# Optimization experiments

Hardware: AMD Instinct MI355X
Metric: run time of the kernel (lower is better)

The kernel has to match this reference:

```python
import jax, jax.numpy as jnp
import numpy as np

D_MODEL = 512
N_HEADS = 8
D_HEAD = D_MODEL // N_HEADS


def setup_inputs() -> dict:
    key = jax.random.key(0)
    ks = jax.random.split(key, 11)
    B, T = 4, 2048
    s = 1.0 / np.sqrt(D_MODEL)
    inp = {
        "Q": jax.random.normal(ks[0], (B, T, D_MODEL), jnp.float32),
        "K": jax.random.normal(ks[1], (B, T, D_MODEL), jnp.float32),
        "V": jax.random.normal(ks[2], (B, T, D_MODEL), jnp.float32),
        "W_q": jax.random.normal(ks[3], (D_MODEL, D_MODEL), jnp.float32) * s,
        "b_q": jnp.zeros((D_MODEL,), jnp.float32),
        "W_k": jax.random.normal(ks[4], (D_MODEL, D_MODEL), jnp.float32) * s,
        "b_k": jnp.zeros((D_MODEL,), jnp.float32),
        "W_v": jax.random.normal(ks[5], (D_MODEL, D_MODEL), jnp.float32) * s,
        "b_v": jnp.zeros((D_MODEL,), jnp.float32),
        "W_o": jax.random.normal(ks[6], (D_MODEL, D_MODEL), jnp.float32) * s,
        "b_o": jnp.zeros((D_MODEL,), jnp.float32),
    }
    return inp


def reference(Q, K, V, W_q, b_q, W_k, b_k, W_v, b_v, W_o, b_o):
    B, Tq, _ = Q.shape
    Tk = K.shape[1]
    # projections (torch Linear: x @ W.T + b)
    q = (Q @ W_q.T + b_q).reshape(B, Tq, N_HEADS, D_HEAD).transpose(0, 2, 1, 3)
    k = (K @ W_k.T + b_k).reshape(B, Tk, N_HEADS, D_HEAD).transpose(0, 2, 1, 3)
    v = (V @ W_v.T + b_v).reshape(B, Tk, N_HEADS, D_HEAD).transpose(0, 2, 1, 3)
    # scaled dot-product attention (mask=None path)
    scores = jnp.einsum("bhqd,bhkd->bhqk", q, k) / np.sqrt(D_HEAD).astype(np.float32)
    attn = jax.nn.softmax(scores, axis=-1)
    ctx = jnp.einsum("bhqk,bhkd->bhqd", attn, v)  # (B,h,Tq,d_v)
    ctx = ctx.transpose(0, 2, 1, 3).reshape(B, Tq, D_MODEL)
    out = ctx @ W_o.T + b_o
    return out, attn
```

## Files before the change

### kernel.cpp

```cpp
#include <hip/hip_runtime.h>
#include <math.h>

#define T_SEQ 2048
#define DM 512
#define NH 8
#define BATCH 4

typedef _Float16 f16;
typedef _Float16 f16x8 __attribute__((ext_vector_type(8)));
typedef _Float16 f16x4 __attribute__((ext_vector_type(4)));
typedef float f32x4 __attribute__((ext_vector_type(4)));

__device__ __forceinline__ f32x4 mfma16(f16x8 a, f16x8 b, f32x4 c) {
    return __builtin_amdgcn_mfma_f32_16x16x32_f16(a, b, c, 0, 0, 0);
}

__device__ __forceinline__ void cvt_f16x16(const float4& x0, const float4& x1,
                                           const float4& x2, const float4& x3,
                                           f16* dst) {
    f16x8 h0, h1;
    h0[0] = x0.x; h0[1] = x0.y; h0[2] = x0.z; h0[3] = x0.w;
    h0[4] = x1.x; h0[5] = x1.y; h0[6] = x1.z; h0[7] = x1.w;
    h1[0] = x2.x; h1[1] = x2.y; h1[2] = x2.z; h1[3] = x2.w;
    h1[4] = x3.x; h1[5] = x3.y; h1[6] = x3.z; h1[7] = x3.w;
    *(f16x8*)dst = h0; *(f16x8*)(dst + 8) = h1;
}

template <int XMODE, int OUTMODE>
__global__ __launch_bounds__(256)
void proj_kernel(const void* __restrict__ Xv, const float* __restrict__ W,
                 const float* __restrict__ bias, void* __restrict__ outv,
                 float scale)
{
    __shared__ char smem[18432];
    f16 (*As)[72] = (f16(*)[72])smem;
    f16 (*Bs)[72] = (f16(*)[72])(smem + 9216);

    const int tid  = threadIdx.x;
    const int lane = tid & 63;
    const int w    = tid >> 6;
    const int m    = lane & 15;
    const int quad = lane >> 4;
    const int m_off = (w & 1) * 32;
    const int n_off = (w >> 1) * 32;
    const int m0 = blockIdx.x << 6;
    const int n0 = blockIdx.y << 6;

    const int r = tid >> 2;
    const int c = (tid & 3) << 4;

    f32x4 acc[2][2] = {};

    const float* wrow = W + (size_t)(n0 + r) * 512 + c;

    float4 ax0, ax1, ax2, ax3;
    f16x8  ah0, ah1;
    float4 bx0, bx1, bx2, bx3;

    if (XMODE == 0) {
        const float* xr = (const float*)Xv + (size_t)(m0 + r) * 512 + c;
        ax0 = ((const float4*)xr)[0]; ax1 = ((const float4*)xr)[1];
        ax2 = ((const float4*)xr)[2]; ax3 = ((const float4*)xr)[3];
    } else {
        const f16x8* xr = (const f16x8*)((const f16*)Xv + (size_t)(m0 + r) * 512 + c);
        ah0 = xr[0]; ah1 = xr[1];
    }
    bx0 = ((const float4*)wrow)[0]; bx1 = ((const float4*)wrow)[1];
    bx2 = ((const float4*)wrow)[2]; bx3 = ((const float4*)wrow)[3];

    for (int k0 = 0; k0 < 512; k0 += 64) {
        __syncthreads();
        if (XMODE == 0) {
            cvt_f16x16(ax0, ax1, ax2, ax3, &As[r][c]);
        } else {
            *(f16x8*)&As[r][c] = ah0; *(f16x8*)&As[r][c + 8] = ah1;
        }
        cvt_f16x16(bx0, bx1, bx2, bx3, &Bs[r][c]);
        if (k0 + 64 < 512) {
            if (XMODE == 0) {
                const float* xr = (const float*)Xv + (size_t)(m0 + r) * 512 + k0 + 64 + c;
                ax0 = ((const float4*)xr)[0]; ax1 = ((const float4*)xr)[1];
                ax2 = ((const float4*)xr)[2]; ax3 = ((const float4*)xr)[3];
            } else {
                const f16x8* xr = (const f16x8*)((const f16*)Xv +
                                  (size_t)(m0 + r) * 512 + k0 + 64 + c);
                ah0 = xr[0]; ah1 = xr[1];
            }
            const float* wr2 = wrow + k0 + 64;
            bx0 = ((const float4*)wr2)[0]; bx1 = ((const float4*)wr2)[1];
            bx2 = ((const float4*)wr2)[2]; bx3 = ((const float4*)wr2)[3];
        }
        __syncthreads();

#pragma unroll
        for (int kk = 0; kk < 64; kk += 32) {
            f16x8 a0 = *(const f16x8*)&As[m_off + m][kk + quad * 8];
            f16x8 a1 = *(const f16x8*)&As[m_off + 16 + m][kk + quad * 8];
            f16x8 b0 = *(const f16x8*)&Bs[n_off + m][kk + quad * 8];
            f16x8 b1 = *(const f16x8*)&Bs[n_off + 16 + m][kk + quad * 8];
            acc[0][0] = mfma16(a0, b0, acc[0][0]);
            acc[0][1] = mfma16(a0, b1, acc[0][1]);
            acc[1][0] = mfma16(a1, b0, acc[1][0]);
            acc[1][1] = mfma16(a1, b1, acc[1][1]);
        }
    }

    float biasn[2];
    biasn[0] = bias[n0 + n_off + m];
    biasn[1] = bias[n0 + n_off + 16 + m];

    const int b = m0 >> 11;
    const int h = n0 >> 6;

    if (OUTMODE == 0) {
        __syncthreads();
        f16 (*Cs16)[72] = (f16(*)[72])smem;
#pragma unroll
        for (int bm = 0; bm < 2; ++bm)
#pragma unroll
            for (int bn = 0; bn < 2; ++bn)
#pragma unroll
                for (int reg = 0; reg < 4; ++reg)
                    Cs16[m_off + bm * 16 + quad * 4 + reg][n_off + bn * 16 + m] =
                        (f16)((acc[bm][bn][reg] + biasn[bn]) * scale);
        __syncthreads();
        f16* outp = (f16*)outv;
        const size_t row = ((size_t)(b * NH + h) * T_SEQ + ((m0 + r) & 2047)) * 64 + c;
        *(f16x8*)&outp[row]     = *(const f16x8*)&Cs16[r][c];
        *(f16x8*)&outp[row + 8] = *(const f16x8*)&Cs16[r][c + 8];
    } else if (OUTMODE == 1) {
        f16* vt = (f16*)outv;
#pragma unroll
        for (int bm = 0; bm < 2; ++bm)
#pragma unroll
            for (int bn = 0; bn < 2; ++bn) {
                const int tg = (m0 + m_off + bm * 16 + quad * 4) & 2047;
                const int dd = n_off + bn * 16 + m;
                f16x4 v4;
#pragma unroll
                for (int reg = 0; reg < 4; ++reg)
                    v4[reg] = (f16)(acc[bm][bn][reg] + biasn[bn]);
                *(f16x4*)&vt[((size_t)(b * NH + h) * 64 + dd) * T_SEQ + tg] = v4;
            }
    } else {
        __syncthreads();
        float (*Cs)[68] = (float(*)[68])smem;
#pragma unroll
        for (int bm = 0; bm < 2; ++bm)
#pragma unroll
            for (int bn = 0; bn < 2; ++bn)
#pragma unroll
                for (int reg = 0; reg < 4; ++reg)
                    Cs[m_off + bm * 16 + quad * 4 + reg][n_off + bn * 16 + m] =
                        acc[bm][bn][reg] + biasn[bn];
        __syncthreads();
        float* outp = (float*)outv + (size_t)(m0 + r) * 512 + n0 + c;
        ((float4*)outp)[0] = *(const float4*)&Cs[r][c];
        ((float4*)outp)[1] = *(const float4*)&Cs[r][c + 4];
        ((float4*)outp)[2] = *(const float4*)&Cs[r][c + 8];
        ((float4*)outp)[3] = *(const float4*)&Cs[r][c + 12];
    }
}

__global__ __launch_bounds__(256)
void attn_kernel(const f16* __restrict__ qh, const f16* __restrict__ kh,
                 const f16* __restrict__ vt, float* __restrict__ attn,
                 f16* __restrict__ ctx)
{
    __shared__ f16 q_s[64][72];
    __shared__ f16 k_s[64][72];
    __shared__ f16 vt_s[64][72];
    __shared__ f16 p_s[4][16][72];

    const int tid  = threadIdx.x;
    const int lane = tid & 63;
    const int w    = tid >> 6;
    const int m    = lane & 15;
    const int quad = lane >> 4;
    const int bh   = blockIdx.y;
    const int i0   = blockIdx.x << 6;

    const int r = tid >> 2;
    const int c = (tid & 3) << 4;

    {
        const f16x8* src = (const f16x8*)&qh[((size_t)bh * T_SEQ + i0 + r) * 64 + c];
        *(f16x8*)&q_s[r][c] = src[0]; *(f16x8*)&q_s[r][c + 8] = src[1];
    }

    const f16* kbase = &kh[((size_t)bh * T_SEQ + r) * 64 + c];
    const f16* vbase = &vt[((size_t)bh * 64 + r) * T_SEQ + c];

    f16x8 kr0 = ((const f16x8*)kbase)[0];
    f16x8 kr1 = ((const f16x8*)kbase)[1];

    float lsum[4] = {0.f, 0.f, 0.f, 0.f};

#pragma unroll 1
    for (int j0 = 0; j0 < T_SEQ; j0 += 64) {
        __syncthreads();
        *(f16x8*)&k_s[r][c] = kr0; *(f16x8*)&k_s[r][c + 8] = kr1;
        if (j0 + 64 < T_SEQ) {
            const f16x8* nk = (const f16x8*)(kbase + (size_t)(j0 + 64) * 64);
            kr0 = nk[0]; kr1 = nk[1];
        }
        __syncthreads();

        f32x4 s[4] = {};
#pragma unroll
        for (int kk = 0; kk < 64; kk += 32) {
            f16x8 a = *(const f16x8*)&q_s[w * 16 + m][kk + quad * 8];
#pragma unroll
            for (int bn = 0; bn < 4; ++bn) {
                f16x8 b = *(const f16x8*)&k_s[bn * 16 + m][kk + quad * 8];
                s[bn] = mfma16(a, b, s[bn]);
            }
        }
#pragma unroll
        for (int reg = 0; reg < 4; ++reg)
            lsum[reg] += __expf(s[0][reg]) + __expf(s[1][reg]) +
                         __expf(s[2][reg]) + __expf(s[3][reg]);
    }

    float inv_l[4];
#pragma unroll
    for (int reg = 0; reg < 4; ++reg) {
        float t = lsum[reg];
        t += __shfl_xor(t, 1);
        t += __shfl_xor(t, 2);
        t += __shfl_xor(t, 4);
        t += __shfl_xor(t, 8);
        inv_l[reg] = 1.0f / t;
    }

    f32x4 o[4] = {};
    kr0 = ((const f16x8*)kbase)[0];
    kr1 = ((const f16x8*)kbase)[1];
    f16x8 vr0 = ((const f16x8*)vbase)[0];
    f16x8 vr1 = ((const f16x8*)vbase)[1];

#pragma unroll 1
    for (int j0 = 0; j0 < T_SEQ; j0 += 64) {
        __syncthreads();
        *(f16x8*)&k_s[r][c]  = kr0; *(f16x8*)&k_s[r][c + 8]  = kr1;
        *(f16x8*)&vt_s[r][c] = vr0; *(f16x8*)&vt_s[r][c + 8] = vr1;
        if (j0 + 64 < T_SEQ) {
            const f16x8* nk = (const f16x8*)(kbase + (size_t)(j0 + 64) * 64);
            kr0 = nk[0]; kr1 = nk[1];
            const f16x8* nv = (const f16x8*)(vbase + j0 + 64);
            vr0 = nv[0]; vr1 = nv[1];
        }
        __syncthreads();

        f32x4 s[4] = {};
#pragma unroll
        for (int kk = 0; kk < 64; kk += 32) {
            f16x8 a = *(const f16x8*)&q_s[w * 16 + m][kk + quad * 8];
#pragma unroll
            for (int bn = 0; bn < 4; ++bn) {
                f16x8 b = *(const f16x8*)&k_s[bn * 16 + m][kk + quad * 8];
                s[bn] = mfma16(a, b, s[bn]);
            }
        }

        const size_t arow_base = ((size_t)bh * T_SEQ + i0 + w * 16 + quad * 4) * T_SEQ + j0;
#pragma unroll
        for (int reg = 0; reg < 4; ++reg) {
            float* arow = attn + arow_base + (size_t)reg * T_SEQ;
#pragma unroll
            for (int bn = 0; bn < 4; ++bn) {
                const float p = __expf(s[bn][reg]) * inv_l[reg];
                arow[bn * 16 + m] = p;
                p_s[w][quad * 4 + reg][bn * 16 + m] = (f16)p;
            }
        }

#pragma unroll
        for (int kk = 0; kk < 64; kk += 32) {
            f16x8 pa = *(const f16x8*)&p_s[w][m][kk + quad * 8];
#pragma unroll
            for (int bd = 0; bd < 4; ++bd) {
                f16x8 vb = *(const f16x8*)&vt_s[bd * 16 + m][kk + quad * 8];
                o[bd] = mfma16(pa, vb, o[bd]);
            }
        }
    }

    __syncthreads();
#pragma unroll
    for (int bd = 0; bd < 4; ++bd)
#pragma unroll
        for (int reg = 0; reg < 4; ++reg)
            q_s[w * 16 + quad * 4 + reg][bd * 16 + m] = (f16)(o[bd][reg]);
    __syncthreads();

    const int b = bh >> 3, h = bh & 7;
    const size_t row = ((size_t)b * T_SEQ + i0 + r) * 512 + h * 64 + c;
    *(f16x8*)&ctx[row]     = *(const f16x8*)&q_s[r][c];
    *(f16x8*)&ctx[row + 8] = *(const f16x8*)&q_s[r][c + 8];
}

extern "C" void kernel_launch(void* const* d_in, const int* in_sizes, int n_in,
                              void* d_out, int out_size, void* d_ws, size_t ws_size,
                              hipStream_t stream) {
    const float* Q   = (const float*)d_in[0];
    const float* K   = (const float*)d_in[1];
    const float* V   = (const float*)d_in[2];
    const float* W_q = (const float*)d_in[3];
    const float* b_q = (const float*)d_in[4];
    const float* W_k = (const float*)d_in[5];
    const float* b_k = (const float*)d_in[6];
    const float* W_v = (const float*)d_in[7];
    const float* b_v = (const float*)d_in[8];
    const float* W_o = (const float*)d_in[9];
    const float* b_o = (const float*)d_in[10];

    float* out  = (float*)d_out;
    float* attn = out + (size_t)BATCH * T_SEQ * DM;

    const size_t HSZ = (size_t)BATCH * NH * T_SEQ * 64;
    f16* qh   = (f16*)d_ws;
    f16* khp  = qh + HSZ;
    f16* vtp  = khp + HSZ;
    f16* ctxh = vtp + HSZ;

    const dim3 blk(256);
    const dim3 gProj(128, 8);

    proj_kernel<0, 0><<<gProj, blk, 0, stream>>>(Q, W_q, b_q, qh, 0.125f);
    proj_kernel<0, 0><<<gProj, blk, 0, stream>>>(K, W_k, b_k, khp, 1.0f);
    proj_kernel<0, 1><<<gProj, blk, 0, stream>>>(V, W_v, b_v, vtp, 1.0f);

    attn_kernel<<<dim3(32, 32), blk, 0, stream>>>(qh, khp, vtp, attn, ctxh);

    proj_kernel<1, 2><<<gProj, blk, 0, stream>>>(ctxh, W_o, b_o, out, 1.0f);
}
```

Baseline: 734.3 us.

## Double-buffer K/V tiles and enlarge attention blocks to 128 query rows

The attention kernel now uses 512 threads covering 128 query rows per block, so each K/V tile loaded into shared memory serves twice as many queries. K and V tiles are double-buffered in shared memory with a register prefetch two tiles ahead, which cuts the per-iteration barriers from two to one. The aim is to reduce K/V reload traffic and barrier stalls. In exchange the kernel uses more shared memory per block and the grid has half as many blocks.

```diff
diff --git a/kernel.cpp b/kernel.cpp
--- a/kernel.cpp
+++ b/kernel.cpp
@@ -162,15 +162,15 @@
     }
 }
 
-__global__ __launch_bounds__(256)
+__global__ __launch_bounds__(512, 4)
 void attn_kernel(const f16* __restrict__ qh, const f16* __restrict__ kh,
                  const f16* __restrict__ vt, float* __restrict__ attn,
                  f16* __restrict__ ctx)
 {
-    __shared__ f16 q_s[64][72];
-    __shared__ f16 k_s[64][72];
-    __shared__ f16 vt_s[64][72];
-    __shared__ f16 p_s[4][16][72];
+    __shared__ f16 q_s[128][72];
+    __shared__ f16 kbuf[2][64][72];
+    __shared__ f16 vbuf[2][64][72];
+    __shared__ f16 p_s[8][16][72];
 
     const int tid  = threadIdx.x;
     const int lane = tid & 63;
@@ -178,48 +178,49 @@
     const int m    = lane & 15;
     const int quad = lane >> 4;
     const int bh   = blockIdx.y;
-    const int i0   = blockIdx.x << 6;
-
-    const int r = tid >> 2;
-    const int c = (tid & 3) << 4;
+    const int i0   = blockIdx.x << 7;
+
+    const int qr = tid >> 2;
+    const int qc = (tid & 3) << 4;
+    const int sr = tid >> 3;
+    const int sc = (tid & 7) << 3;
 
     {
-        const f16x8* src = (const f16x8*)&qh[((size_t)bh * T_SEQ + i0 + r) * 64 + c];
-        *(f16x8*)&q_s[r][c] = src[0]; *(f16x8*)&q_s[r][c + 8] = src[1];
-    }
-
-    const f16* kbase = &kh[((size_t)bh * T_SEQ + r) * 64 + c];
-    const f16* vbase = &vt[((size_t)bh * 64 + r) * T_SEQ + c];
-
-    f16x8 kr0 = ((const f16x8*)kbase)[0];
-    f16x8 kr1 = ((const f16x8*)kbase)[1];
+        const f16x8* src = (const f16x8*)&qh[((size_t)bh * T_SEQ + i0 + qr) * 64 + qc];
+        *(f16x8*)&q_s[qr][qc] = src[0]; *(f16x8*)&q_s[qr][qc + 8] = src[1];
+    }
+
+    const f16* kbase = &kh[((size_t)bh * T_SEQ + sr) * 64 + sc];
+    const f16* vbase = &vt[((size_t)bh * 64 + sr) * T_SEQ + sc];
 
     float lsum[4] = {0.f, 0.f, 0.f, 0.f};
+    {
+        f16x8 kr = *(const f16x8*)kbase;
+        *(f16x8*)&kbuf[0][sr][sc] = kr;
+        kr = *(const f16x8*)(kbase + (size_t)64 * 64);
 
 #pragma unroll 1
-    for (int j0 = 0; j0 < T_SEQ; j0 += 64) {
-        __syncthreads();
-        *(f16x8*)&k_s[r][c] = kr0; *(f16x8*)&k_s[r][c + 8] = kr1;
-        if (j0 + 64 < T_SEQ) {
-            const f16x8* nk = (const f16x8*)(kbase + (size_t)(j0 + 64) * 64);
-            kr0 = nk[0]; kr1 = nk[1];
-        }
-        __syncthreads();
-
-        f32x4 s[4] = {};
-#pragma unroll
-        for (int kk = 0; kk < 64; kk += 32) {
-            f16x8 a = *(const f16x8*)&q_s[w * 16 + m][kk + quad * 8];
-#pragma unroll
-            for (int bn = 0; bn < 4; ++bn) {
-                f16x8 b = *(const f16x8*)&k_s[bn * 16 + m][kk + quad * 8];
-                s[bn] = mfma16(a, b, s[bn]);
-            }
-        }
-#pragma unroll
-        for (int reg = 0; reg < 4; ++reg)
-            lsum[reg] += __expf(s[0][reg]) + __expf(s[1][reg]) +
-                         __expf(s[2][reg]) + __expf(s[3][reg]);
+        for (int j = 0; j < 32; ++j) {
+            __syncthreads();
+            if (j + 1 < 32) *(f16x8*)&kbuf[(j + 1) & 1][sr][sc] = kr;
+            if (j + 2 < 32) kr = *(const f16x8*)(kbase + (size_t)(j + 2) * 64 * 64);
+
+            const f16 (*ks)[72] = kbuf[j & 1];
+            f32x4 s[4] = {};
+#pragma unroll
+            for (int kk = 0; kk < 64; kk += 32) {
+                f16x8 a = *(const f16x8*)&q_s[w * 16 + m][kk + quad * 8];
+#pragma unroll
+                for (int bn = 0; bn < 4; ++bn) {
+                    f16x8 b = *(const f16x8*)&ks[bn * 16 + m][kk + quad * 8];
+                    s[bn] = mfma16(a, b, s[bn]);
+                }
+            }
+#pragma unroll
+            for (int reg = 0; reg < 4; ++reg)
+                lsum[reg] += __expf(s[0][reg]) + __expf(s[1][reg]) +
+                             __expf(s[2][reg]) + __expf(s[3][reg]);
+        }
     }
 
     float inv_l[4];
@@ -234,54 +235,63 @@
     }
 
     f32x4 o[4] = {};
-    kr0 = ((const f16x8*)kbase)[0];
-    kr1 = ((const f16x8*)kbase)[1];
-    f16x8 vr0 = ((const f16x8*)vbase)[0];
-    f16x8 vr1 = ((const f16x8*)vbase)[1];
+    {
+        __syncthreads();
+        f16x8 kr = *(const f16x8*)kbase;
+        f16x8 vr = *(const f16x8*)vbase;
+        *(f16x8*)&kbuf[0][sr][sc] = kr;
+        *(f16x8*)&vbuf[0][sr][sc] = vr;
+        kr = *(const f16x8*)(kbase + (size_t)64 * 64);
+        vr = *(const f16x8*)(vbase + 64);
 
 #pragma unroll 1
-    for (int j0 = 0; j0 < T_SEQ; j0 += 64) {
-        __syncthreads();
-        *(f16x8*)&k_s[r][c]  = kr0; *(f16x8*)&k_s[r][c + 8]  = kr1;
-        *(f16x8*)&vt_s[r][c] = vr0; *(f16x8*)&vt_s[r][c + 8] = vr1;
-        if (j0 + 64 < T_SEQ) {
-            const f16x8* nk = (const f16x8*)(kbase + (size_t)(j0 + 64) * 64);
-            kr0 = nk[0]; kr1 = nk[1];
-            const f16x8* nv = (const f16x8*)(vbase + j0 + 64);
-            vr0 = nv[0]; vr1 = nv[1];
-        }
-        __syncthreads();
-
-        f32x4 s[4] = {};
-#pragma unroll
-        for (int kk = 0; kk < 64; kk += 32) {
-            f16x8 a = *(const f16x8*)&q_s[w * 16 + m][kk + quad * 8];
-#pragma unroll
-            for (int bn = 0; bn < 4; ++bn) {
-                f16x8 b = *(const f16x8*)&k_s[bn * 16 + m][kk + quad * 8];
-                s[bn] = mfma16(a, b, s[bn]);
-            }
-        }
-
-        const size_t arow_base = ((size_t)bh * T_SEQ + i0 + w * 16 + quad * 4) * T_SEQ + j0;
-#pragma unroll
-        for (int reg = 0; reg < 4; ++reg) {
-            float* arow = attn + arow_base + (size_t)reg * T_SEQ;
-#pragma unroll
-            for (int bn = 0; bn < 4; ++bn) {
-                const float p = __expf(s[bn][reg]) * inv_l[reg];
-                arow[bn * 16 + m] = p;
-                p_s[w][quad * 4 + reg][bn * 16 + m] = (f16)p;
-            }
-        }
-
-#pragma unroll
-        for (int kk = 0; kk < 64; kk += 32) {
-            f16x8 pa = *(const f16x8*)&p_s[w][m][kk + quad * 8];
-#pragma unroll
-            for (int bd = 0; bd < 4; ++bd) {
-                f16x8 vb = *(const f16x8*)&vt_s[bd * 16 + m][kk + quad * 8];
-                o[bd] = mfma16(pa, vb, o[bd]);
+        for (int j = 0; j < 32; ++j) {
+            const int j0 = j << 6;
+            __syncthreads();
+            if (j + 1 < 32) {
+                *(f16x8*)&kbuf[(j + 1) & 1][sr][sc] = kr;
+                *(f16x8*)&vbuf[(j + 1) & 1][sr][sc] = vr;
+            }
+            if (j + 2 < 32) {
+                kr = *(const f16x8*)(kbase + (size_t)(j + 2) * 64 * 64);
+                vr = *(const f16x8*)(vbase + (j + 2) * 64);
+            }
+
+            const f16 (*ks)[72] = kbuf[j & 1];
+            const f16 (*vs)[72] = vbuf[j & 1];
+
+            f32x4 s[4] = {};
+#pragma unroll
+            for (int kk = 0; kk < 64; kk += 32) {
+                f16x8 a = *(const f16x8*)&q_s[w * 16 + m][kk + quad * 8];
+#pragma unroll
+                for (int bn = 0; bn < 4; ++bn) {
+                    f16x8 b = *(const f16x8*)&ks[bn * 16 + m][kk + quad * 8];
+                    s[bn] = mfma16(a, b, s[bn]);
+                }
+            }
+
+            const size_t arow_base =
+                ((size_t)bh * T_SEQ + i0 + w * 16 + quad * 4) * T_SEQ + j0;
+#pragma unroll
+            for (int reg = 0; reg < 4; ++reg) {
+                float* arow = attn + arow_base + (size_t)reg * T_SEQ;
+#pragma unroll
+                for (int bn = 0; bn < 4; ++bn) {
+                    const float p = __expf(s[bn][reg]) * inv_l[reg];
+                    arow[bn * 16 + m] = p;
+                    p_s[w][quad * 4 + reg][bn * 16 + m] = (f16)p;
+                }
+            }
+
+#pragma unroll
+            for (int kk = 0; kk < 64; kk += 32) {
+                f16x8 pa = *(const f16x8*)&p_s[w][m][kk + quad * 8];
+#pragma unroll
+                for (int bd = 0; bd < 4; ++bd) {
+                    f16x8 vb = *(const f16x8*)&vs[bd * 16 + m][kk + quad * 8];
+                    o[bd] = mfma16(pa, vb, o[bd]);
+                }
             }
         }
     }
@@ -295,9 +305,9 @@
     __syncthreads();
 
     const int b = bh >> 3, h = bh & 7;
-    const size_t row = ((size_t)b * T_SEQ + i0 + r) * 512 + h * 64 + c;
-    *(f16x8*)&ctx[row]     = *(const f16x8*)&q_s[r][c];
-    *(f16x8*)&ctx[row + 8] = *(const f16x8*)&q_s[r][c + 8];
+    const size_t row = ((size_t)b * T_SEQ + i0 + qr) * 512 + h * 64 + qc;
+    *(f16x8*)&ctx[row]     = *(const f16x8*)&q_s[qr][qc];
+    *(f16x8*)&ctx[row + 8] = *(const f16x8*)&q_s[qr][qc + 8];
 }
 
 extern "C" void kernel_launch(void* const* d_in, const int* in_sizes, int n_in,
@@ -331,7 +341,7 @@
     proj_kernel<0, 0><<<gProj, blk, 0, stream>>>(K, W_k, b_k, khp, 1.0f);
     proj_kernel<0, 1><<<gProj, blk, 0, stream>>>(V, W_v, b_v, vtp, 1.0f);
 
-    attn_kernel<<<dim3(32, 32), blk, 0, stream>>>(qh, khp, vtp, attn, ctxh);
+    attn_kernel<<<dim3(16, 32), dim3(512), 0, stream>>>(qh, khp, vtp, attn, ctxh);
 
     proj_kernel<1, 2><<<gProj, blk, 0, stream>>>(ctxh, W_o, b_o, out, 1.0f);
 }
```

New measurement: 734.8 us. No clear change (+0.1%).
